# Performance work log

Measured on AMD Instinct MI355X. Metric: run time of the kernel, lower is better.

Reference implementation:

```python
import jax, jax.numpy as jnp
import numpy as np

N_DRUG, N_DIS, D = 8000, 18000, 128
N_REL_DIR, E = 3, 200000  # 3 forward dd etypes + 3 reverse etypes


def setup_inputs() -> dict:
    key = jax.random.key(0)
    ks = jax.random.split(key, 7)
    return {
        "h_drug": jax.random.normal(ks[0], (N_DRUG, D), dtype=jnp.float32),
        "h_disease": jax.random.normal(ks[1], (N_DIS, D), dtype=jnp.float32),
        "W": jax.random.normal(ks[2], (2 * N_REL_DIR, D), dtype=jnp.float32),
        "drug_src": jax.random.randint(ks[3], (N_REL_DIR, E), 0, N_DRUG, dtype=jnp.int32),
        "dis_dst": jax.random.randint(ks[4], (N_REL_DIR, E), 0, N_DIS, dtype=jnp.int32),
        "dis_src": jax.random.randint(ks[5], (N_REL_DIR, E), 0, N_DIS, dtype=jnp.int32),
        "drug_dst": jax.random.randint(ks[6], (N_REL_DIR, E), 0, N_DRUG, dtype=jnp.int32),
    }


def reference(h_drug, h_disease, W, drug_src, dis_dst, dis_src, drug_dst):
    # DistMult apply_edges per etype: score = sigmoid(sum(h_u * W[rel] * h_v, -1))
    # Relations 0..2: drug -> disease; relations 3..5: disease -> drug (reverse).
    W_fwd, W_rev = W[:N_REL_DIR], W[N_REL_DIR:]  # [3, d] each
    # gather-multiply-reduce over [rel, edge, d]
    s_fwd = jnp.einsum("red,rd,red->re", h_drug[drug_src], W_fwd, h_disease[dis_dst])
    s_rev = jnp.einsum("red,rd,red->re", h_disease[dis_src], W_rev, h_drug[drug_dst])
    scores = jnp.concatenate([s_fwd, s_rev], axis=0)  # [6, E]
    return jax.nn.sigmoid(scores)
```

## Files before the change

### kernel.cpp

```cpp
#include <hip/hip_runtime.h>
#include <hip/hip_fp16.h>
#include <math.h>

#define NREL    3
#define EDGES   200000
#define DIM     128
#define PASSES  5
#define UNITS   6250
#define BJ      313
#define JPER    (6 * BJ)

#define NDRUG   8000
#define NDIS    18000
#define DRUG_ELEMS (NDRUG * DIM)
#define TOT_ELEMS  ((NDRUG + NDIS) * DIM)

typedef _Float16 half8 __attribute__((ext_vector_type(8)));

__global__ __launch_bounds__(256) void convert_fp16(
    const float* __restrict__ drug, const float* __restrict__ dis,
    _Float16* __restrict__ o)
{
    const int i = blockIdx.x * 256 + threadIdx.x;
    const int nd8 = DRUG_ELEMS / 8, nt8 = TOT_ELEMS / 8;
    if (i >= nt8) return;
    const float4* s; int j;
    if (i < nd8) { s = (const float4*)drug; j = i * 2; }
    else         { s = (const float4*)dis;  j = (i - nd8) * 2; }
    const float4 x = s[j], y = s[j + 1];
    half8 h;
    h[0] = (_Float16)x.x; h[1] = (_Float16)x.y;
    h[2] = (_Float16)x.z; h[3] = (_Float16)x.w;
    h[4] = (_Float16)y.x; h[5] = (_Float16)y.y;
    h[6] = (_Float16)y.z; h[7] = (_Float16)y.w;
    ((half8*)o)[i] = h;
}

__global__ __launch_bounds__(256, 4) void distmult_fp16(
    const _Float16* __restrict__ tabs,
    const float* __restrict__ W,
    const int* __restrict__ drug_src, const int* __restrict__ dis_dst,
    const int* __restrict__ dis_src,  const int* __restrict__ drug_dst,
    float* __restrict__ part0,
    float* __restrict__ part1)
{
    const int b     = blockIdx.x;
    const int slot  = b & 7;
    const int chunk = slot >> 2;
    const int q     = slot & 3;
    const int j     = b >> 3;
    const int ro    = j / BJ;
    const int bj    = j % BJ;

    const int eg   = threadIdx.x >> 3;
    const int lane = threadIdx.x & 7;

    const _Float16* tabD = tabs;
    const _Float16* tabS = tabs + DRUG_ELEMS;
    const _Float16 *tabA, *tabB; const int *idxA, *idxB;
    if (ro < NREL) {
        tabA = tabD; tabB = tabS;
        idxA = drug_src + ro * EDGES;
        idxB = dis_dst  + ro * EDGES;
    } else {
        tabA = tabS; tabB = tabD;
        idxA = dis_src  + (ro - NREL) * EDGES;
        idxB = drug_dst + (ro - NREL) * EDGES;
    }

    const int off = chunk * 64 + lane * 8;
    const _Float16* tA = tabA + off;
    const _Float16* tB = tabB + off;
    float* pbase = (chunk == 0 ? part0 : part1) + (size_t)ro * EDGES;

    int e[PASSES];
    bool valid[PASSES];
    int ia[PASSES], ib[PASSES];
    #pragma unroll
    for (int p = 0; p < PASSES; ++p) {
        const int u = q + 4 * (p + PASSES * bj);
        valid[p] = (u < UNITS);
        const int uc = valid[p] ? u : (UNITS - 1);
        e[p] = uc * 32 + eg;
        asm volatile("global_load_dword %0, %1, off"
                     : "=v"(ia[p]) : "v"(idxA + e[p]));
        asm volatile("global_load_dword %0, %1, off"
                     : "=v"(ib[p]) : "v"(idxB + e[p]));
    }

    float4 wlo, whi;
    asm volatile("global_load_dwordx4 %0, %1, off"
                 : "=v"(wlo) : "v"(W + ro * DIM + off));
    asm volatile("global_load_dwordx4 %0, %1, off"
                 : "=v"(whi) : "v"(W + ro * DIM + off + 4));

    asm volatile("s_waitcnt vmcnt(2)");
    __builtin_amdgcn_sched_barrier(0);

    half8 a8[PASSES], b8[PASSES];
    #pragma unroll
    for (int p = 0; p < PASSES; ++p) {
        asm volatile("global_load_dwordx4 %0, %1, off"
                     : "=v"(a8[p]) : "v"(tA + ia[p] * DIM));
        asm volatile("global_load_dwordx4 %0, %1, off"
                     : "=v"(b8[p]) : "v"(tB + ib[p] * DIM));
    }

    float res[PASSES];

#define DOT(p)                                                              \
    {                                                                       \
        float s = 0.0f;                                                     \
        s = fmaf((float)a8[p][0] * (float)b8[p][0], wlo.x, s);              \
        s = fmaf((float)a8[p][1] * (float)b8[p][1], wlo.y, s);              \
        s = fmaf((float)a8[p][2] * (float)b8[p][2], wlo.z, s);              \
        s = fmaf((float)a8[p][3] * (float)b8[p][3], wlo.w, s);              \
        s = fmaf((float)a8[p][4] * (float)b8[p][4], whi.x, s);              \
        s = fmaf((float)a8[p][5] * (float)b8[p][5], whi.y, s);              \
        s = fmaf((float)a8[p][6] * (float)b8[p][6], whi.z, s);              \
        s = fmaf((float)a8[p][7] * (float)b8[p][7], whi.w, s);              \
        s += __shfl_xor(s, 4, 64);                                          \
        s += __shfl_xor(s, 2, 64);                                          \
        s += __shfl_xor(s, 1, 64);                                          \
        res[p] = s;                                                         \
    }

    asm volatile("s_waitcnt vmcnt(8)");
    __builtin_amdgcn_sched_barrier(0);
    DOT(0)
    asm volatile("s_waitcnt vmcnt(6)");
    __builtin_amdgcn_sched_barrier(0);
    DOT(1)
    asm volatile("s_waitcnt vmcnt(4)");
    __builtin_amdgcn_sched_barrier(0);
    DOT(2)
    asm volatile("s_waitcnt vmcnt(2)");
    __builtin_amdgcn_sched_barrier(0);
    DOT(3)
    asm volatile("s_waitcnt vmcnt(0)");
    __builtin_amdgcn_sched_barrier(0);
    DOT(4)
#undef DOT

    if (lane == 0) {
        #pragma unroll
        for (int p = 0; p < PASSES; ++p)
            if (valid[p])
                __builtin_nontemporal_store(res[p], pbase + e[p]);
    }
}

__global__ __launch_bounds__(256) void reduce_sigmoid(
    const float* __restrict__ part1, float* __restrict__ out)
{
    const int i = blockIdx.x * 256 + threadIdx.x;
    if (i >= (6 * EDGES) / 4) return;
    float4 v = ((const float4*)out)[i];
    const float4 a = ((const float4*)part1)[i];
    v.x = 1.0f / (1.0f + __expf(-(v.x + a.x)));
    v.y = 1.0f / (1.0f + __expf(-(v.y + a.y)));
    v.z = 1.0f / (1.0f + __expf(-(v.z + a.z)));
    v.w = 1.0f / (1.0f + __expf(-(v.w + a.w)));
    ((float4*)out)[i] = v;
}

__global__ __launch_bounds__(256) void distmult_atomic(
    const float* __restrict__ h_drug, const float* __restrict__ h_disease,
    const float* __restrict__ W,
    const int* __restrict__ drug_src, const int* __restrict__ dis_dst,
    const int* __restrict__ dis_src, const int* __restrict__ drug_dst,
    float* __restrict__ out)
{
    const int b = blockIdx.x;
    const int slot = b & 7, chunk = slot >> 1, half = slot & 1;
    const int j = b >> 3;
    const int ro = j / 625, batch = j % 625;
    const int eg = threadIdx.x >> 3, lane = threadIdx.x & 7;

    const float* tabA; const float* tabB;
    const int* idxA; const int* idxB;
    if (ro < NREL) {
        tabA = h_drug;    tabB = h_disease;
        idxA = drug_src + (size_t)ro * EDGES;
        idxB = dis_dst  + (size_t)ro * EDGES;
    } else {
        tabA = h_disease; tabB = h_drug;
        idxA = dis_src  + (size_t)(ro - NREL) * EDGES;
        idxB = drug_dst + (size_t)(ro - NREL) * EDGES;
    }
    const int off = chunk * 32;
    const float4 w4 = ((const float4*)(W + (size_t)ro * DIM + off))[lane];

    #pragma unroll
    for (int p = 0; p < 5; ++p) {
        const int e = batch * 320 + p * 64 + half * 32 + eg;
        const int ia = __builtin_nontemporal_load(idxA + e);
        const int ib = __builtin_nontemporal_load(idxB + e);
        const float4 a4 = ((const float4*)(tabA + (size_t)ia * DIM + off))[lane];
        const float4 b4 = ((const float4*)(tabB + (size_t)ib * DIM + off))[lane];
        float s = a4.x * w4.x * b4.x + a4.y * w4.y * b4.y
                + a4.z * w4.z * b4.z + a4.w * w4.w * b4.w;
        s += __shfl_xor(s, 4, 64);
        s += __shfl_xor(s, 2, 64);
        s += __shfl_xor(s, 1, 64);
        if (lane == 0) atomicAdd(&out[(size_t)ro * EDGES + e], s);
    }
}

__global__ __launch_bounds__(256) void sigmoid_inplace(float* __restrict__ out)
{
    const int i = blockIdx.x * 256 + threadIdx.x;
    if (i >= (6 * EDGES) / 4) return;
    float4 v = ((float4*)out)[i];
    v.x = 1.0f / (1.0f + __expf(-v.x));
    v.y = 1.0f / (1.0f + __expf(-v.y));
    v.z = 1.0f / (1.0f + __expf(-v.z));
    v.w = 1.0f / (1.0f + __expf(-v.w));
    ((float4*)out)[i] = v;
}

extern "C" void kernel_launch(void* const* d_in, const int* in_sizes, int n_in,
                              void* d_out, int out_size, void* d_ws, size_t ws_size,
                              hipStream_t stream) {
    const float* h_drug    = (const float*)d_in[0];
    const float* h_disease = (const float*)d_in[1];
    const float* W         = (const float*)d_in[2];
    const int*   drug_src  = (const int*)d_in[3];
    const int*   dis_dst   = (const int*)d_in[4];
    const int*   dis_src   = (const int*)d_in[5];
    const int*   drug_dst  = (const int*)d_in[6];
    float*       out       = (float*)d_out;

    const int n4 = (6 * EDGES) / 4;
    const size_t tab_bytes = (size_t)TOT_ELEMS * 2;
    const size_t ws_need   = tab_bytes + (size_t)6 * EDGES * sizeof(float);

    if (ws_size >= ws_need) {
        _Float16* tabs  = (_Float16*)d_ws;
        float*    part1 = (float*)((char*)d_ws + tab_bytes);

        convert_fp16<<<(TOT_ELEMS / 8 + 255) / 256, 256, 0, stream>>>(
            h_drug, h_disease, tabs);
        distmult_fp16<<<8 * JPER, 256, 0, stream>>>(
            tabs, W, drug_src, dis_dst, dis_src, drug_dst, out, part1);
        reduce_sigmoid<<<(n4 + 255) / 256, 256, 0, stream>>>(part1, out);
    } else {
        (void)hipMemsetAsync(out, 0, (size_t)6 * EDGES * sizeof(float), stream);
        distmult_atomic<<<8 * 6 * 625, 256, 0, stream>>>(
            h_drug, h_disease, W, drug_src, dis_dst, dis_src, drug_dst, out);
        sigmoid_inplace<<<(n4 + 255) / 256, 256, 0, stream>>>(out);
    }
}
```

Before: 115.5 us.

## Fuse convert, gather-dot and sigmoid into one cooperative persistent kernel

Replaces the three separate launches (fp16 table conversion, gather-multiply-reduce, partial-sum sigmoid) with one cooperative kernel of 1024 blocks. The stages are separated by grid-wide syncs, and the persistent blocks loop over the virtual block indices. This is meant to remove per-launch gaps and tail effects between stages, at the cost of two grid barriers and fewer resident blocks during the gather phase. Partial-result stores also change from nontemporal builtins to plain inline-asm global stores, which may keep them cached for the final pass. If the cooperative launch fails, the code falls back to the original three launches.

```diff
diff --git a/kernel.cpp b/kernel.cpp
--- a/kernel.cpp
+++ b/kernel.cpp
@@ -1,6 +1,9 @@
 #include <hip/hip_runtime.h>
 #include <hip/hip_fp16.h>
+#include <hip/hip_cooperative_groups.h>
 #include <math.h>
+
+namespace cg = cooperative_groups;
 
 #define NREL    3
 #define EDGES   200000
@@ -9,6 +12,7 @@
 #define UNITS   6250
 #define BJ      313
 #define JPER    (6 * BJ)
+#define VBLOCKS (8 * JPER)
 
 #define NDRUG   8000
 #define NDIS    18000
@@ -17,38 +21,17 @@
 
 typedef _Float16 half8 __attribute__((ext_vector_type(8)));
 
-__global__ __launch_bounds__(256) void convert_fp16(
-    const float* __restrict__ drug, const float* __restrict__ dis,
-    _Float16* __restrict__ o)
-{
-    const int i = blockIdx.x * 256 + threadIdx.x;
-    const int nd8 = DRUG_ELEMS / 8, nt8 = TOT_ELEMS / 8;
-    if (i >= nt8) return;
-    const float4* s; int j;
-    if (i < nd8) { s = (const float4*)drug; j = i * 2; }
-    else         { s = (const float4*)dis;  j = (i - nd8) * 2; }
-    const float4 x = s[j], y = s[j + 1];
-    half8 h;
-    h[0] = (_Float16)x.x; h[1] = (_Float16)x.y;
-    h[2] = (_Float16)x.z; h[3] = (_Float16)x.w;
-    h[4] = (_Float16)y.x; h[5] = (_Float16)y.y;
-    h[6] = (_Float16)y.z; h[7] = (_Float16)y.w;
-    ((half8*)o)[i] = h;
-}
-
-__global__ __launch_bounds__(256, 4) void distmult_fp16(
-    const _Float16* __restrict__ tabs,
-    const float* __restrict__ W,
+__device__ __forceinline__ void distmult_body(
+    int vb,
+    const _Float16* __restrict__ tabs, const float* __restrict__ W,
     const int* __restrict__ drug_src, const int* __restrict__ dis_dst,
     const int* __restrict__ dis_src,  const int* __restrict__ drug_dst,
-    float* __restrict__ part0,
-    float* __restrict__ part1)
-{
-    const int b     = blockIdx.x;
-    const int slot  = b & 7;
+    float* __restrict__ part0, float* __restrict__ part1)
+{
+    const int slot  = vb & 7;
     const int chunk = slot >> 2;
     const int q     = slot & 3;
-    const int j     = b >> 3;
+    const int j     = vb >> 3;
     const int ro    = j / BJ;
     const int bj    = j % BJ;
 
@@ -107,7 +90,6 @@
     }
 
     float res[PASSES];
-
 #define DOT(p)                                                              \
     {                                                                       \
         float s = 0.0f;                                                     \
@@ -124,7 +106,6 @@
         s += __shfl_xor(s, 1, 64);                                          \
         res[p] = s;                                                         \
     }
-
     asm volatile("s_waitcnt vmcnt(8)");
     __builtin_amdgcn_sched_barrier(0);
     DOT(0)
@@ -146,8 +127,86 @@
         #pragma unroll
         for (int p = 0; p < PASSES; ++p)
             if (valid[p])
-                __builtin_nontemporal_store(res[p], pbase + e[p]);
-    }
+                asm volatile("global_store_dword %0, %1, off"
+                             :: "v"(pbase + e[p]), "v"(res[p]));
+    }
+}
+
+__global__ __launch_bounds__(256, 4) void fused_all(
+    const float* __restrict__ drug, const float* __restrict__ dis,
+    const float* __restrict__ W,
+    const int* __restrict__ drug_src, const int* __restrict__ dis_dst,
+    const int* __restrict__ dis_src,  const int* __restrict__ drug_dst,
+    _Float16* __restrict__ tabs, float* __restrict__ part1,
+    float* __restrict__ out)
+{
+    cg::grid_group grid = cg::this_grid();
+    const int tid = blockIdx.x * 256 + threadIdx.x;
+    const int nthr = gridDim.x * 256;
+
+    {
+        const int nd8 = DRUG_ELEMS / 8, nt8 = TOT_ELEMS / 8;
+        for (int i = tid; i < nt8; i += nthr) {
+            const float4* s; int j;
+            if (i < nd8) { s = (const float4*)drug; j = i * 2; }
+            else         { s = (const float4*)dis;  j = (i - nd8) * 2; }
+            const float4 x = s[j], y = s[j + 1];
+            half8 h;
+            h[0] = (_Float16)x.x; h[1] = (_Float16)x.y;
+            h[2] = (_Float16)x.z; h[3] = (_Float16)x.w;
+            h[4] = (_Float16)y.x; h[5] = (_Float16)y.y;
+            h[6] = (_Float16)y.z; h[7] = (_Float16)y.w;
+            ((half8*)tabs)[i] = h;
+        }
+    }
+    grid.sync();
+
+    for (int vb = blockIdx.x; vb < VBLOCKS; vb += gridDim.x)
+        distmult_body(vb, tabs, W, drug_src, dis_dst, dis_src, drug_dst,
+                      out, part1);
+    grid.sync();
+
+    {
+        const int n4 = (6 * EDGES) / 4;
+        for (int i = tid; i < n4; i += nthr) {
+            float4 v = ((const float4*)out)[i];
+            const float4 a = ((const float4*)part1)[i];
+            v.x = 1.0f / (1.0f + __expf(-(v.x + a.x)));
+            v.y = 1.0f / (1.0f + __expf(-(v.y + a.y)));
+            v.z = 1.0f / (1.0f + __expf(-(v.z + a.z)));
+            v.w = 1.0f / (1.0f + __expf(-(v.w + a.w)));
+            ((float4*)out)[i] = v;
+        }
+    }
+}
+
+__global__ __launch_bounds__(256) void convert_fp16(
+    const float* __restrict__ drug, const float* __restrict__ dis,
+    _Float16* __restrict__ o)
+{
+    const int i = blockIdx.x * 256 + threadIdx.x;
+    const int nd8 = DRUG_ELEMS / 8, nt8 = TOT_ELEMS / 8;
+    if (i >= nt8) return;
+    const float4* s; int j;
+    if (i < nd8) { s = (const float4*)drug; j = i * 2; }
+    else         { s = (const float4*)dis;  j = (i - nd8) * 2; }
+    const float4 x = s[j], y = s[j + 1];
+    half8 h;
+    h[0] = (_Float16)x.x; h[1] = (_Float16)x.y;
+    h[2] = (_Float16)x.z; h[3] = (_Float16)x.w;
+    h[4] = (_Float16)y.x; h[5] = (_Float16)y.y;
+    h[6] = (_Float16)y.z; h[7] = (_Float16)y.w;
+    ((half8*)o)[i] = h;
+}
+
+__global__ __launch_bounds__(256, 4) void distmult_fp16(
+    const _Float16* __restrict__ tabs, const float* __restrict__ W,
+    const int* __restrict__ drug_src, const int* __restrict__ dis_dst,
+    const int* __restrict__ dis_src,  const int* __restrict__ drug_dst,
+    float* __restrict__ part0, float* __restrict__ part1)
+{
+    distmult_body(blockIdx.x, tabs, W, drug_src, dis_dst, dis_src, drug_dst,
+                  part0, part1);
 }
 
 __global__ __launch_bounds__(256) void reduce_sigmoid(
@@ -239,11 +298,20 @@
         _Float16* tabs  = (_Float16*)d_ws;
         float*    part1 = (float*)((char*)d_ws + tab_bytes);
 
-        convert_fp16<<<(TOT_ELEMS / 8 + 255) / 256, 256, 0, stream>>>(
-            h_drug, h_disease, tabs);
-        distmult_fp16<<<8 * JPER, 256, 0, stream>>>(
-            tabs, W, drug_src, dis_dst, dis_src, drug_dst, out, part1);
-        reduce_sigmoid<<<(n4 + 255) / 256, 256, 0, stream>>>(part1, out);
+        void* args[] = { (void*)&h_drug, (void*)&h_disease, (void*)&W,
+                         (void*)&drug_src, (void*)&dis_dst,
+                         (void*)&dis_src, (void*)&drug_dst,
+                         (void*)&tabs, (void*)&part1, (void*)&out };
+        hipError_t err = hipLaunchCooperativeKernel(
+            (const void*)fused_all, dim3(1024), dim3(256), args, 0, stream);
+
+        if (err != hipSuccess) {
+            convert_fp16<<<(TOT_ELEMS / 8 + 255) / 256, 256, 0, stream>>>(
+                h_drug, h_disease, tabs);
+            distmult_fp16<<<VBLOCKS, 256, 0, stream>>>(
+                tabs, W, drug_src, dis_dst, dis_src, drug_dst, out, part1);
+            reduce_sigmoid<<<(n4 + 255) / 256, 256, 0, stream>>>(part1, out);
+        }
     } else {
         (void)hipMemsetAsync(out, 0, (size_t)6 * EDGES * sizeof(float), stream);
         distmult_atomic<<<8 * 6 * 625, 256, 0, stream>>>(
```

New measurement: 393.6 us. +240.9%, slower.

## Compute full 128-dim dot per edge and fuse sigmoid, dropping partial reduction kernel

Applied to the files above, without the earlier changes.

Each edge's dot product is now handled by 16 lanes covering all 128 dimensions instead of being split into two 64-dim halves written to separate partial buffers. The sigmoid is applied inside the main kernel, so the separate reduce_sigmoid pass and the partial-sum workspace buffer are no longer needed. This saves one kernel launch and a full read/write pass over the 6x200000 output, and halves the index loads per edge. The cost is one extra shuffle step per dot, and each block now covers 16 edges per pass instead of 32 with the same grid size.

```diff
diff --git a/kernel.cpp b/kernel.cpp
--- a/kernel.cpp
+++ b/kernel.cpp
@@ -6,9 +6,9 @@
 #define EDGES   200000
 #define DIM     128
 #define PASSES  5
-#define UNITS   6250
-#define BJ      313
-#define JPER    (6 * BJ)
+#define UNITS2  12500
+#define BJ2     313
+#define VBLOCKS (8 * 6 * BJ2)
 
 #define NDRUG   8000
 #define NDIS    18000
@@ -36,24 +36,21 @@
     ((half8*)o)[i] = h;
 }
 
-__global__ __launch_bounds__(256, 4) void distmult_fp16(
+__global__ __launch_bounds__(256, 4) void distmult_full(
     const _Float16* __restrict__ tabs,
     const float* __restrict__ W,
     const int* __restrict__ drug_src, const int* __restrict__ dis_dst,
     const int* __restrict__ dis_src,  const int* __restrict__ drug_dst,
-    float* __restrict__ part0,
-    float* __restrict__ part1)
-{
-    const int b     = blockIdx.x;
-    const int slot  = b & 7;
-    const int chunk = slot >> 2;
-    const int q     = slot & 3;
-    const int j     = b >> 3;
-    const int ro    = j / BJ;
-    const int bj    = j % BJ;
-
-    const int eg   = threadIdx.x >> 3;
-    const int lane = threadIdx.x & 7;
+    float* __restrict__ out)
+{
+    const int b    = blockIdx.x;
+    const int q    = b & 7;
+    const int j    = b >> 3;
+    const int ro   = j / BJ2;
+    const int bj   = j % BJ2;
+
+    const int eg   = threadIdx.x >> 4;
+    const int lane = threadIdx.x & 15;
 
     const _Float16* tabD = tabs;
     const _Float16* tabS = tabs + DRUG_ELEMS;
@@ -68,20 +65,20 @@
         idxB = drug_dst + (ro - NREL) * EDGES;
     }
 
-    const int off = chunk * 64 + lane * 8;
+    const int off = lane * 8;
     const _Float16* tA = tabA + off;
     const _Float16* tB = tabB + off;
-    float* pbase = (chunk == 0 ? part0 : part1) + (size_t)ro * EDGES;
+    float* obase = out + (size_t)ro * EDGES;
 
     int e[PASSES];
     bool valid[PASSES];
     int ia[PASSES], ib[PASSES];
     #pragma unroll
     for (int p = 0; p < PASSES; ++p) {
-        const int u = q + 4 * (p + PASSES * bj);
-        valid[p] = (u < UNITS);
-        const int uc = valid[p] ? u : (UNITS - 1);
-        e[p] = uc * 32 + eg;
+        const int u = q + 8 * (p + PASSES * bj);
+        valid[p] = (u < UNITS2);
+        const int uc = valid[p] ? u : (UNITS2 - 1);
+        e[p] = uc * 16 + eg;
         asm volatile("global_load_dword %0, %1, off"
                      : "=v"(ia[p]) : "v"(idxA + e[p]));
         asm volatile("global_load_dword %0, %1, off"
@@ -107,7 +104,6 @@
     }
 
     float res[PASSES];
-
 #define DOT(p)                                                              \
     {                                                                       \
         float s = 0.0f;                                                     \
@@ -119,12 +115,12 @@
         s = fmaf((float)a8[p][5] * (float)b8[p][5], whi.y, s);              \
         s = fmaf((float)a8[p][6] * (float)b8[p][6], whi.z, s);              \
         s = fmaf((float)a8[p][7] * (float)b8[p][7], whi.w, s);              \
+        s += __shfl_xor(s, 8, 64);                                          \
         s += __shfl_xor(s, 4, 64);                                          \
         s += __shfl_xor(s, 2, 64);                                          \
         s += __shfl_xor(s, 1, 64);                                          \
         res[p] = s;                                                         \
     }
-
     asm volatile("s_waitcnt vmcnt(8)");
     __builtin_amdgcn_sched_barrier(0);
     DOT(0)
@@ -145,23 +141,11 @@
     if (lane == 0) {
         #pragma unroll
         for (int p = 0; p < PASSES; ++p)
-            if (valid[p])
-                __builtin_nontemporal_store(res[p], pbase + e[p]);
-    }
-}
-
-__global__ __launch_bounds__(256) void reduce_sigmoid(
-    const float* __restrict__ part1, float* __restrict__ out)
-{
-    const int i = blockIdx.x * 256 + threadIdx.x;
-    if (i >= (6 * EDGES) / 4) return;
-    float4 v = ((const float4*)out)[i];
-    const float4 a = ((const float4*)part1)[i];
-    v.x = 1.0f / (1.0f + __expf(-(v.x + a.x)));
-    v.y = 1.0f / (1.0f + __expf(-(v.y + a.y)));
-    v.z = 1.0f / (1.0f + __expf(-(v.z + a.z)));
-    v.w = 1.0f / (1.0f + __expf(-(v.w + a.w)));
-    ((float4*)out)[i] = v;
+            if (valid[p]) {
+                const float v = 1.0f / (1.0f + __expf(-res[p]));
+                __builtin_nontemporal_store(v, obase + e[p]);
+            }
+    }
 }
 
 __global__ __launch_bounds__(256) void distmult_atomic(
@@ -233,17 +217,14 @@
 
     const int n4 = (6 * EDGES) / 4;
     const size_t tab_bytes = (size_t)TOT_ELEMS * 2;
-    const size_t ws_need   = tab_bytes + (size_t)6 * EDGES * sizeof(float);
-
-    if (ws_size >= ws_need) {
-        _Float16* tabs  = (_Float16*)d_ws;
-        float*    part1 = (float*)((char*)d_ws + tab_bytes);
+
+    if (ws_size >= tab_bytes) {
+        _Float16* tabs = (_Float16*)d_ws;
 
         convert_fp16<<<(TOT_ELEMS / 8 + 255) / 256, 256, 0, stream>>>(
             h_drug, h_disease, tabs);
-        distmult_fp16<<<8 * JPER, 256, 0, stream>>>(
-            tabs, W, drug_src, dis_dst, dis_src, drug_dst, out, part1);
-        reduce_sigmoid<<<(n4 + 255) / 256, 256, 0, stream>>>(part1, out);
+        distmult_full<<<VBLOCKS, 256, 0, stream>>>(
+            tabs, W, drug_src, dis_dst, dis_src, drug_dst, out);
     } else {
         (void)hipMemsetAsync(out, 0, (size_t)6 * EDGES * sizeof(float), stream);
         distmult_atomic<<<8 * 6 * 625, 256, 0, stream>>>(
```

New measurement: 119.0 us. 3.1% more time.
